# Optimization experiments

Measured on AMD Instinct MI355X. Metric: run time of the kernel, lower is better.

## Reference

```python
import jax, jax.numpy as jnp
import numpy as np

MAX_ITER = 10
EPS = 0.01


def setup_inputs() -> dict:
    key = jax.random.key(0)
    ks = jax.random.split(key, 6)
    B, D, H, O = 4096, 512, 1024, 512
    return {
        "x": jax.random.normal(ks[0], (B, D), jnp.float32),
        "prev_hidden": jax.random.normal(ks[1], (B, H), jnp.float32) * 0.1,
        "prev_ponder": jnp.zeros((B, 1), jnp.float32),
        "prev_steps": jnp.zeros((B, 1), jnp.float32),
        "W_ih": jax.random.normal(ks[2], (H, D + 1), jnp.float32) * 0.02,
        "b_ih": jnp.zeros((H,), jnp.float32),
        "W_hh": jax.random.normal(ks[3], (H, H), jnp.float32) * 0.02,
        "b_hh": jnp.zeros((H,), jnp.float32),
        "W_halt": jax.random.normal(ks[4], (1, H), jnp.float32) * 0.1,
        "b_halt": jnp.zeros((1,), jnp.float32),
        "W_ans": jax.random.normal(ks[5], (O, H), jnp.float32) * 0.02,
        "b_ans": jnp.zeros((O,), jnp.float32),
    }


def reference(x, prev_hidden, prev_ponder, prev_steps,
              W_ih, b_ih, W_hh, b_hh, W_halt, b_halt, W_ans, b_ans):
    B = x.shape[0]
    O = W_ans.shape[0]

    def controller(x_n, s):  # vanilla tanh RNN cell (cfg.MODEL.LSTM=False)
        return jnp.tanh(x_n @ W_ih.T + b_ih + s @ W_hh.T + b_hh)

    def halting_step(carry, inp):
        flag, n = inp  # n is the 1-based loop index (float), flag=1 only at n==1
        s_n, s_acc, y, h, r_n, R, N, steps = carry
        x_n = jnp.concatenate([x, jnp.full((B, 1), flag, x.dtype)], axis=1)
        s_new = controller(x_n, s_n)                       # [B, H]
        h_n = jax.nn.sigmoid(s_new @ W_halt.T + b_halt)    # [B, 1]
        y_n = s_new @ W_ans.T + b_ans                      # [B, O]
        h = h + h_n
        isN = h >= (1.0 - EPS)                             # halted mask (frozen once true)
        p_n = jnp.where(isN, r_n, h_n)                     # remainder at halting step, else h_n
        y = y + p_n * y_n
        s_acc = s_acc + p_n * s_new
        steps = jnp.where(isN, steps, steps + 1.0)
        r_new = jnp.where(isN, jnp.zeros((), x.dtype), 1.0 - h)
        R_new = jnp.where(isN, R, r_new)
        N_new = jnp.where(isN, N, n + 1.0)
        return (s_new, s_acc, y, h, r_new, R_new, N_new, steps), None

    carry0 = (
        prev_hidden,                          # s_n
        jnp.zeros_like(prev_hidden),          # s accumulator
        jnp.zeros((B, O), x.dtype),           # y
        jnp.zeros((B, 1), x.dtype),           # h (halt prob mass)
        jnp.ones((B, 1), x.dtype),            # r_n
        jnp.ones((B, 1), x.dtype),            # R
        jnp.zeros((B, 1), x.dtype),           # N
        prev_steps + 1.0,                     # steps
    )
    ns = jnp.arange(1, MAX_ITER, dtype=x.dtype)
    flags = (ns == 1).astype(x.dtype)
    carry, _ = jax.lax.scan(halting_step, carry0, (flags, ns))
    s_n, s_acc, y, h, r_n, R, N, steps = carry

    # final (remainder) step, flag = 1 only if MAX_ITER == 1
    final_flag = 1.0 if MAX_ITER == 1 else 0.0
    x_n = jnp.concatenate([x, jnp.full((B, 1), final_flag, x.dtype)], axis=1)
    s_new = controller(x_n, s_n)
    y_n = s_new @ W_ans.T + b_ans
    p_n = r_n                                 # remainder (0 for already-halted rows)
    y = y + p_n * y_n
    s_acc = s_acc + p_n * s_new
    ponder_cost = prev_ponder + R + N
    return (y, s_acc, ponder_cost, steps)
```

## Files before the change

### kernel.cpp

```cpp
#include <hip/hip_runtime.h>
#include <cmath>
#include <cstddef>


#define MAX_ITER 10

typedef short bf16x8 __attribute__((ext_vector_type(8)));
typedef float f32x4  __attribute__((ext_vector_type(4)));

__device__ __forceinline__ ushort f2bf(float f) {
    unsigned u = __float_as_uint(f);
    u += 0x7fff + ((u >> 16) & 1);
    return (ushort)(u >> 16);
}
__device__ __forceinline__ float bf2f(ushort b) {
    return __uint_as_float(((unsigned)b) << 16);
}
__device__ __forceinline__ void gld16(const void* g, void* l) {
    __builtin_amdgcn_global_load_lds(
        (const __attribute__((address_space(1))) void*)g,
        (__attribute__((address_space(3))) void*)l, 16, 0, 0);
}

template<int BM, int BN, int MODE>
__device__ __forceinline__ void gemm_body(
    int bx, int by,
    const ushort* __restrict__ ahi, const ushort* __restrict__ alo, int lda,
    const ushort* __restrict__ bhi, const ushort* __restrict__ blo, int ldb,
    int tps, float* __restrict__ Cout, int ldn,
    const float* __restrict__ e0, const float* __restrict__ e1, float flag,
    ushort* __restrict__ shiO, ushort* __restrict__ sloO,
    ushort* smem)
{
    constexpr int FRM = BM / 32;
    constexpr int FRN = BN / 32;
    constexpr int NL  = BM / 32 + BN / 32;
    ushort* As = smem;
    ushort* Bs = smem + 2 * BM * 64;

    const int tid  = threadIdx.x;
    const int lane = tid & 63;
    const int wave = tid >> 6;
    const int lq   = lane & 15;
    const int kh   = lane >> 4;
    const int wr0  = (wave >> 1) * (BM / 2);
    const int wc0  = (wave & 1) * (BN / 2);
    const int m0   = bx * BM;
    const int n0   = by * BN;

    f32x4 acc[FRM][FRN];
#pragma unroll
    for (int r = 0; r < FRM; ++r)
#pragma unroll
        for (int c = 0; c < FRN; ++c) acc[r][c] = (f32x4)0.f;

    const int steps = 3 * tps;

    auto stage = [&](int buf, int t) {
        const int seg = (t >= 2 * tps) ? 2 : ((t >= tps) ? 1 : 0);
        const int k0  = (t - seg * tps) * 64;
        const ushort* aS = (seg == 2) ? alo : ahi;
        const ushort* bS = (seg == 1) ? blo : bhi;
#pragma unroll
        for (int j = 0; j < BM / 32; ++j) {
            int c   = j * 256 + tid;
            int row = c >> 3;
            int kb  = ((c & 7) << 4) ^ ((row & 7) << 4);
            gld16(aS + (size_t)(m0 + row) * lda + k0 + (kb >> 1),
                  As + buf * (BM * 64) + (size_t)(j * 256 + (tid & ~63)) * 8);
        }
#pragma unroll
        for (int j = 0; j < BN / 32; ++j) {
            int c   = j * 256 + tid;
            int row = c >> 3;
            int kb  = ((c & 7) << 4) ^ ((row & 7) << 4);
            gld16(bS + (size_t)(n0 + row) * ldb + k0 + (kb >> 1),
                  Bs + buf * (BN * 64) + (size_t)(j * 256 + (tid & ~63)) * 8);
        }
    };

    stage(0, 0);
    stage(1, 1);

    int cur = 0;
    for (int t = 0; t < steps; ++t) {
        if (t + 1 < steps) __builtin_amdgcn_s_waitcnt(0xF70 | NL);
        else               __builtin_amdgcn_s_waitcnt(0xF70);
        __builtin_amdgcn_sched_barrier(0);
        __builtin_amdgcn_s_barrier();
        __builtin_amdgcn_sched_barrier(0);

        const ushort* Ab = As + cur * (BM * 64);
        const ushort* Bb = Bs + cur * (BN * 64);
#pragma unroll
        for (int kt = 0; kt < 2; ++kt) {
            bf16x8 af[FRM], bfr[FRN];
#pragma unroll
            for (int r = 0; r < FRM; ++r) {
                int row = wr0 + r * 16 + lq;
                int kb  = (kt * 64 + kh * 16) ^ ((row & 7) << 4);
                af[r] = *reinterpret_cast<const bf16x8*>(&Ab[row * 64 + (kb >> 1)]);
            }
#pragma unroll
            for (int c = 0; c < FRN; ++c) {
                int row = wc0 + c * 16 + lq;
                int kb  = (kt * 64 + kh * 16) ^ ((row & 7) << 4);
                bfr[c] = *reinterpret_cast<const bf16x8*>(&Bb[row * 64 + (kb >> 1)]);
            }
            __builtin_amdgcn_s_setprio(1);
#pragma unroll
            for (int r = 0; r < FRM; ++r)
#pragma unroll
                for (int c = 0; c < FRN; ++c)
                    acc[r][c] = __builtin_amdgcn_mfma_f32_16x16x32_bf16(
                        af[r], bfr[c], acc[r][c], 0, 0, 0);
            __builtin_amdgcn_s_setprio(0);
        }
        __builtin_amdgcn_sched_barrier(0);
        __builtin_amdgcn_s_barrier();
        __builtin_amdgcn_sched_barrier(0);
        if (t + 2 < steps) stage(cur, t + 2);
        cur ^= 1;
    }

#pragma unroll
    for (int r = 0; r < FRM; ++r)
#pragma unroll
        for (int c = 0; c < FRN; ++c) {
            const size_t col = n0 + wc0 + c * 16 + lq;
#pragma unroll
            for (int q = 0; q < 4; ++q) {
                const size_t row = m0 + wr0 + r * 16 + kh * 4 + q;
                float v = acc[r][c][q];
                if constexpr (MODE == 0) {
                    v += e0[col] + e1[col];
                    Cout[row * ldn + col] = v;
                } else if constexpr (MODE == 1) {
                    v += e0[row * ldn + col];
                    if (flag != 0.f) v += flag * e1[col];
                    float s = tanhf(v);
                    ushort hb = f2bf(s);
                    ushort lb = f2bf(s - bf2f(hb));
                    shiO[row * ldn + col] = hb;
                    sloO[row * ldn + col] = lb;
                } else {
                    const float pv = e1[row];
                    float* cp = &Cout[row * ldn + col];
                    *cp = fmaf(pv, v + e0[col], *cp);
                }
            }
        }
}

template<int BM, int BN, int MODE>
__global__ __launch_bounds__(256)
void mfma_gemm(const ushort* __restrict__ ahi, const ushort* __restrict__ alo, int lda,
               const ushort* __restrict__ bhi, const ushort* __restrict__ blo, int ldb,
               int tps, float* __restrict__ Cout, int ldn,
               const float* __restrict__ e0, const float* __restrict__ e1,
               float flag, ushort* __restrict__ shiO, ushort* __restrict__ sloO)
{
    __shared__ __align__(16) ushort smem[2 * (BM + BN) * 64];
    gemm_body<BM, BN, MODE>(blockIdx.x, blockIdx.y, ahi, alo, lda, bhi, blo, ldb,
                            tps, Cout, ldn, e0, e1, flag, shiO, sloO, smem);
}

__global__ __launch_bounds__(256)
void merged_gemm(int m1_blocks, int m1_gx, int m2_gx,
                 const ushort* __restrict__ s_hi, const ushort* __restrict__ s_lo,
                 const ushort* __restrict__ whhhi, const ushort* __restrict__ whhlo,
                 int H, int tps,
                 float* __restrict__ xproj, const float* __restrict__ wcol,
                 ushort* __restrict__ o_hi, ushort* __restrict__ o_lo,
                 const ushort* __restrict__ wanshi, const ushort* __restrict__ wanslo,
                 float* __restrict__ out_y, int O,
                 const float* __restrict__ bans, const float* __restrict__ pA)
{
    extern __shared__ ushort smem[];
    const int b = blockIdx.x;
    if (b < m1_blocks) {
        gemm_body<64, 128, 1>(b % m1_gx, b / m1_gx, s_hi, s_lo, H,
                              whhhi, whhlo, H, tps, nullptr, H,
                              xproj, wcol, 0.f, o_hi, o_lo, smem);
    } else {
        const int b2 = b - m1_blocks;
        gemm_body<64, 64, 2>(b2 % m2_gx, b2 / m2_gx, s_hi, s_lo, H,
                             wanshi, wanslo, H, tps, out_y, O,
                             bans, pA, 0.f, nullptr, nullptr, smem);
    }
}

__global__ void init_kernel(float* __restrict__ out_zero, size_t nzero,
                            float* __restrict__ hA, float* __restrict__ rA,
                            float* __restrict__ RA, float* __restrict__ NA,
                            float* __restrict__ stA,
                            const float* __restrict__ prev_steps, int B)
{
    size_t i = (size_t)blockIdx.x * 256 + threadIdx.x;
    if (i < nzero) out_zero[i] = 0.f;
    if (i < (size_t)B) {
        hA[i] = 0.f; rA[i] = 1.f; RA[i] = 1.f; NA[i] = 0.f;
        stA[i] = prev_steps[i] + 1.f;
    }
}

__global__ void split_f32(const float* __restrict__ src,
                          ushort* __restrict__ hi, ushort* __restrict__ lo, size_t n4)
{
    size_t i = (size_t)blockIdx.x * 256 + threadIdx.x;
    if (i < n4) {
        float4 v = reinterpret_cast<const float4*>(src)[i];
        ushort4 h, l;
        h.x = f2bf(v.x); l.x = f2bf(v.x - bf2f(h.x));
        h.y = f2bf(v.y); l.y = f2bf(v.y - bf2f(h.y));
        h.z = f2bf(v.z); l.z = f2bf(v.z - bf2f(h.z));
        h.w = f2bf(v.w); l.w = f2bf(v.w - bf2f(h.w));
        reinterpret_cast<ushort4*>(hi)[i] = h;
        reinterpret_cast<ushort4*>(lo)[i] = l;
    }
}

__global__ void wih_split(const float* __restrict__ Wih,
                          ushort* __restrict__ hi, ushort* __restrict__ lo,
                          float* __restrict__ wcol, int H, int D)
{
    size_t i = (size_t)blockIdx.x * 256 + threadIdx.x;
    if (i < (size_t)H * D) {
        int h = (int)(i / D), d = (int)(i % D);
        float v = Wih[(size_t)h * (D + 1) + d];
        ushort hb = f2bf(v);
        hi[i] = hb; lo[i] = f2bf(v - bf2f(hb));
    }
    if (i < (size_t)H) wcol[i] = Wih[i * (size_t)(D + 1) + D];
}

__global__ __launch_bounds__(256)
void halt_update(const ushort* __restrict__ shi, const ushort* __restrict__ slo,
                 const float* __restrict__ Whalt, const float* __restrict__ bhalt,
                 float* __restrict__ hA, float* __restrict__ rA, float* __restrict__ RA,
                 float* __restrict__ NA, float* __restrict__ stA, float* __restrict__ pA,
                 float* __restrict__ s_acc, float n1, int H, int isFinal)
{
    const int b = blockIdx.x;
    const int tid = threadIdx.x;
    const size_t base = (size_t)b * H;
    const int i = tid * 4;
    ushort4 h4 = *reinterpret_cast<const ushort4*>(shi + base + i);
    ushort4 l4 = *reinterpret_cast<const ushort4*>(slo + base + i);
    float s0 = bf2f(h4.x) + bf2f(l4.x);
    float s1 = bf2f(h4.y) + bf2f(l4.y);
    float s2 = bf2f(h4.z) + bf2f(l4.z);
    float s3 = bf2f(h4.w) + bf2f(l4.w);

    __shared__ float partial[4];
    __shared__ float psh;
    float4 w4 = *reinterpret_cast<const float4*>(Whalt + i);
    float lsum = s0 * w4.x + s1 * w4.y + s2 * w4.z + s3 * w4.w;
#pragma unroll
    for (int off = 32; off > 0; off >>= 1) lsum += __shfl_down(lsum, off, 64);
    if ((tid & 63) == 0) partial[tid >> 6] = lsum;
    __syncthreads();
    if (tid == 0) {
        float pv;
        if (isFinal) {
            pv = rA[b];
        } else {
            float dot = partial[0] + partial[1] + partial[2] + partial[3] + bhalt[0];
            float h_n = 1.f / (1.f + expf(-dot));
            float hh = hA[b] + h_n;
            bool isN = hh >= 0.99f;
            pv = isN ? rA[b] : h_n;
            float r_new = isN ? 0.f : 1.f - hh;
            if (!isN) { RA[b] = r_new; NA[b] = n1; stA[b] += 1.f; }
            hA[b] = hh; rA[b] = r_new; pA[b] = pv;
        }
        psh = pv;
    }
    __syncthreads();
    const float pv = psh;
    if (pv != 0.f) {
        float4* sac = reinterpret_cast<float4*>(s_acc + base + i);
        float4 o = *sac;
        o.x = fmaf(pv, s0, o.x); o.y = fmaf(pv, s1, o.y);
        o.z = fmaf(pv, s2, o.z); o.w = fmaf(pv, s3, o.w);
        *sac = o;
    }
}

__global__ void finalize_kernel(const float* __restrict__ pp, const float* __restrict__ RA,
                                const float* __restrict__ NA, const float* __restrict__ stA,
                                float* __restrict__ pon, float* __restrict__ stp, int B)
{
    int i = blockIdx.x * 256 + threadIdx.x;
    if (i < B) { pon[i] = pp[i] + RA[i] + NA[i]; stp[i] = stA[i]; }
}

extern "C" void kernel_launch(void* const* d_in, const int* in_sizes, int n_in,
                              void* d_out, int out_size, void* d_ws, size_t ws_size,
                              hipStream_t stream)
{
    const float* x     = (const float*)d_in[0];
    const float* ph    = (const float*)d_in[1];
    const float* pp    = (const float*)d_in[2];
    const float* ps    = (const float*)d_in[3];
    const float* Wih   = (const float*)d_in[4];
    const float* bih   = (const float*)d_in[5];
    const float* Whh   = (const float*)d_in[6];
    const float* bhh   = (const float*)d_in[7];
    const float* Whalt = (const float*)d_in[8];
    const float* bhalt = (const float*)d_in[9];
    const float* Wans  = (const float*)d_in[10];
    const float* bans  = (const float*)d_in[11];

    const int B = in_sizes[2];
    const int H = in_sizes[5];
    const int O = in_sizes[11];
    const int D = in_sizes[0] / B;

    float* out_y   = (float*)d_out;
    float* out_sac = out_y + (size_t)B * O;
    float* out_pon = out_sac + (size_t)B * H;
    float* out_stp = out_pon + B;

    char* w = (char*)d_ws;
    float* xproj = (float*)w;  w += (size_t)B * H * 4;
    ushort* shi[2], *slo[2];
    shi[0] = (ushort*)w; w += (size_t)B * H * 2;
    slo[0] = (ushort*)w; w += (size_t)B * H * 2;
    shi[1] = (ushort*)w; w += (size_t)B * H * 2;
    slo[1] = (ushort*)w; w += (size_t)B * H * 2;
    ushort* whhhi = (ushort*)w; w += (size_t)H * H * 2;
    ushort* whhlo = (ushort*)w; w += (size_t)H * H * 2;
    ushort* wanshi = (ushort*)w; w += (size_t)O * H * 2;
    ushort* wanslo = (ushort*)w; w += (size_t)O * H * 2;
    ushort* wihhi = (ushort*)w; w += (size_t)H * D * 2;
    ushort* wihlo = (ushort*)w; w += (size_t)H * D * 2;
    float* wcol = (float*)w; w += (size_t)H * 4;
    float* hA  = (float*)w; w += (size_t)B * 4;
    float* rA  = (float*)w; w += (size_t)B * 4;
    float* RA  = (float*)w; w += (size_t)B * 4;
    float* NA  = (float*)w; w += (size_t)B * 4;
    float* stA = (float*)w; w += (size_t)B * 4;
    float* pA  = (float*)w; w += (size_t)B * 4;

    ushort* xhi = shi[1];
    ushort* xlo = slo[1];

    const size_t nzero = (size_t)B * (O + H);
    init_kernel<<<(unsigned)((nzero + 255) / 256), 256, 0, stream>>>(
        out_y, nzero, hA, rA, RA, NA, stA, ps, B);

    split_f32<<<(unsigned)(((size_t)B * D / 4 + 255) / 256), 256, 0, stream>>>(x, xhi, xlo, (size_t)B * D / 4);
    split_f32<<<(unsigned)(((size_t)B * H / 4 + 255) / 256), 256, 0, stream>>>(ph, shi[0], slo[0], (size_t)B * H / 4);
    split_f32<<<(unsigned)(((size_t)H * H / 4 + 255) / 256), 256, 0, stream>>>(Whh, whhhi, whhlo, (size_t)H * H / 4);
    split_f32<<<(unsigned)(((size_t)O * H / 4 + 255) / 256), 256, 0, stream>>>(Wans, wanshi, wanslo, (size_t)O * H / 4);
    wih_split<<<(unsigned)(((size_t)H * D + 255) / 256), 256, 0, stream>>>(Wih, wihhi, wihlo, wcol, H, D);

    {
        dim3 g(B / 64, H / 128);
        mfma_gemm<64, 128, 0><<<g, 256, 0, stream>>>(
            xhi, xlo, D, wihhi, wihlo, D, D / 64,
            xproj, H, bih, bhh, 0.f, nullptr, nullptr);
    }

    const int m1_gx = B / 64, m1_gy = H / 128;
    const int m2_gx = B / 64, m2_gy = O / 64;
    const int m1_blocks = m1_gx * m1_gy;
    const int m2_blocks = m2_gx * m2_gy;
    const size_t lds_merged = 2u * (64 + 128) * 64 * sizeof(ushort);

    {
        dim3 g(B / 64, H / 128);
        mfma_gemm<64, 128, 1><<<g, 256, 0, stream>>>(
            shi[0], slo[0], H, whhhi, whhlo, H, H / 64,
            nullptr, H, xproj, wcol, 1.f, shi[1], slo[1]);
    }

    int cur = 1;
    for (int t = 1; t < MAX_ITER; t++) {
        halt_update<<<B, 256, 0, stream>>>(
            shi[cur], slo[cur], Whalt, bhalt, hA, rA, RA, NA, stA, pA,
            out_sac, (float)(t + 1), H, 0);
        merged_gemm<<<m1_blocks + m2_blocks, 256, lds_merged, stream>>>(
            m1_blocks, m1_gx, m2_gx,
            shi[cur], slo[cur], whhhi, whhlo, H, H / 64,
            xproj, wcol, shi[cur ^ 1], slo[cur ^ 1],
            wanshi, wanslo, out_y, O, bans, pA);
        cur ^= 1;
    }

    halt_update<<<B, 256, 0, stream>>>(
        shi[cur], slo[cur], Whalt, bhalt, hA, rA, RA, NA, stA, pA,
        out_sac, 0.f, H, 1);
    {
        dim3 g(B / 64, O / 64);
        mfma_gemm<64, 64, 2><<<g, 256, 0, stream>>>(
            shi[cur], slo[cur], H, wanshi, wanslo, H, H / 64,
            out_y, O, bans, rA, 0.f, nullptr, nullptr);
    }

    finalize_kernel<<<(B + 255) / 256, 256, 0, stream>>>(
        pp, RA, NA, stA, out_pon, out_stp, B);
}
```

Before: 860.2 us.

## Hoist answer projection out of loop via linearity, triple-buffer GEMM, store xproj as bf16 split

Relies on the linearity of the answer head: y = s_acc @ W_ans^T + (sum p) * b_ans. The per-step answer GEMM is dropped from the recurrent loop and a single GEMM on the accumulated state runs at the end, with halt_update accumulating the p sum and emitting a hi/lo bf16 split of s_acc. The GEMM pipeline also goes from double to triple buffering, xproj is stored as a bf16 hi/lo pair instead of fp32, and blocks are remapped in an XCD-aware order. Risks include extra LDS per block lowering occupancy and small numeric differences from the reordered accumulation.

```diff
diff --git a/kernel.cpp b/kernel.cpp
--- a/kernel.cpp
+++ b/kernel.cpp
@@ -29,14 +29,15 @@
     const ushort* __restrict__ bhi, const ushort* __restrict__ blo, int ldb,
     int tps, float* __restrict__ Cout, int ldn,
     const float* __restrict__ e0, const float* __restrict__ e1, float flag,
+    const ushort* __restrict__ uA, const ushort* __restrict__ uB,
     ushort* __restrict__ shiO, ushort* __restrict__ sloO,
     ushort* smem)
 {
     constexpr int FRM = BM / 32;
     constexpr int FRN = BN / 32;
-    constexpr int NL  = BM / 32 + BN / 32;
+    constexpr int NL  = (BM + BN) / 32;
     ushort* As = smem;
-    ushort* Bs = smem + 2 * BM * 64;
+    ushort* Bs = smem + 3 * BM * 64;
 
     const int tid  = threadIdx.x;
     const int lane = tid & 63;
@@ -81,10 +82,13 @@
 
     stage(0, 0);
     stage(1, 1);
+    stage(2, 2);
 
     int cur = 0;
     for (int t = 0; t < steps; ++t) {
-        if (t + 1 < steps) __builtin_amdgcn_s_waitcnt(0xF70 | NL);
+        const int rem = steps - 1 - t;
+        if (rem >= 2)      __builtin_amdgcn_s_waitcnt(0xF70 | (2 * NL));
+        else if (rem == 1) __builtin_amdgcn_s_waitcnt(0xF70 | NL);
         else               __builtin_amdgcn_s_waitcnt(0xF70);
         __builtin_amdgcn_sched_barrier(0);
         __builtin_amdgcn_s_barrier();
@@ -119,8 +123,8 @@
         __builtin_amdgcn_sched_barrier(0);
         __builtin_amdgcn_s_barrier();
         __builtin_amdgcn_sched_barrier(0);
-        if (t + 2 < steps) stage(cur, t + 2);
-        cur ^= 1;
+        if (t + 3 < steps) stage(cur, t + 3);
+        cur = (cur == 2) ? 0 : cur + 1;
     }
 
 #pragma unroll
@@ -134,9 +138,12 @@
                 float v = acc[r][c][q];
                 if constexpr (MODE == 0) {
                     v += e0[col] + e1[col];
-                    Cout[row * ldn + col] = v;
+                    ushort hb = f2bf(v);
+                    ushort lb = f2bf(v - bf2f(hb));
+                    shiO[row * ldn + col] = hb;
+                    sloO[row * ldn + col] = lb;
                 } else if constexpr (MODE == 1) {
-                    v += e0[row * ldn + col];
+                    v += bf2f(uA[row * ldn + col]) + bf2f(uB[row * ldn + col]);
                     if (flag != 0.f) v += flag * e1[col];
                     float s = tanhf(v);
                     ushort hb = f2bf(s);
@@ -144,9 +151,7 @@
                     shiO[row * ldn + col] = hb;
                     sloO[row * ldn + col] = lb;
                 } else {
-                    const float pv = e1[row];
-                    float* cp = &Cout[row * ldn + col];
-                    *cp = fmaf(pv, v + e0[col], *cp);
+                    Cout[row * ldn + col] = v + e1[row] * e0[col];
                 }
             }
         }
@@ -154,53 +159,35 @@
 
 template<int BM, int BN, int MODE>
 __global__ __launch_bounds__(256)
-void mfma_gemm(const ushort* __restrict__ ahi, const ushort* __restrict__ alo, int lda,
+void mfma_gemm(int gx,
+               const ushort* __restrict__ ahi, const ushort* __restrict__ alo, int lda,
                const ushort* __restrict__ bhi, const ushort* __restrict__ blo, int ldb,
                int tps, float* __restrict__ Cout, int ldn,
                const float* __restrict__ e0, const float* __restrict__ e1,
-               float flag, ushort* __restrict__ shiO, ushort* __restrict__ sloO)
-{
-    __shared__ __align__(16) ushort smem[2 * (BM + BN) * 64];
-    gemm_body<BM, BN, MODE>(blockIdx.x, blockIdx.y, ahi, alo, lda, bhi, blo, ldb,
-                            tps, Cout, ldn, e0, e1, flag, shiO, sloO, smem);
-}
-
-__global__ __launch_bounds__(256)
-void merged_gemm(int m1_blocks, int m1_gx, int m2_gx,
-                 const ushort* __restrict__ s_hi, const ushort* __restrict__ s_lo,
-                 const ushort* __restrict__ whhhi, const ushort* __restrict__ whhlo,
-                 int H, int tps,
-                 float* __restrict__ xproj, const float* __restrict__ wcol,
-                 ushort* __restrict__ o_hi, ushort* __restrict__ o_lo,
-                 const ushort* __restrict__ wanshi, const ushort* __restrict__ wanslo,
-                 float* __restrict__ out_y, int O,
-                 const float* __restrict__ bans, const float* __restrict__ pA)
-{
-    extern __shared__ ushort smem[];
+               float flag,
+               const ushort* __restrict__ uA, const ushort* __restrict__ uB,
+               ushort* __restrict__ shiO, ushort* __restrict__ sloO)
+{
+    __shared__ __align__(16) ushort smem[3 * (BM + BN) * 64];
+    const int n = gridDim.x;
     const int b = blockIdx.x;
-    if (b < m1_blocks) {
-        gemm_body<64, 128, 1>(b % m1_gx, b / m1_gx, s_hi, s_lo, H,
-                              whhhi, whhlo, H, tps, nullptr, H,
-                              xproj, wcol, 0.f, o_hi, o_lo, smem);
-    } else {
-        const int b2 = b - m1_blocks;
-        gemm_body<64, 64, 2>(b2 % m2_gx, b2 / m2_gx, s_hi, s_lo, H,
-                             wanshi, wanslo, H, tps, out_y, O,
-                             bans, pA, 0.f, nullptr, nullptr, smem);
-    }
-}
-
-__global__ void init_kernel(float* __restrict__ out_zero, size_t nzero,
+    const int w = (b & 7) * (n >> 3) + (b >> 3);
+    gemm_body<BM, BN, MODE>(w % gx, w / gx, ahi, alo, lda, bhi, blo, ldb,
+                            tps, Cout, ldn, e0, e1, flag, uA, uB,
+                            shiO, sloO, smem);
+}
+
+__global__ void init_kernel(float* __restrict__ sacc_zero, size_t nzero,
                             float* __restrict__ hA, float* __restrict__ rA,
                             float* __restrict__ RA, float* __restrict__ NA,
-                            float* __restrict__ stA,
+                            float* __restrict__ stA, float* __restrict__ pAcc,
                             const float* __restrict__ prev_steps, int B)
 {
     size_t i = (size_t)blockIdx.x * 256 + threadIdx.x;
-    if (i < nzero) out_zero[i] = 0.f;
+    if (i < nzero) sacc_zero[i] = 0.f;
     if (i < (size_t)B) {
         hA[i] = 0.f; rA[i] = 1.f; RA[i] = 1.f; NA[i] = 0.f;
-        stA[i] = prev_steps[i] + 1.f;
+        stA[i] = prev_steps[i] + 1.f; pAcc[i] = 0.f;
     }
 }
 
@@ -238,8 +225,11 @@
 void halt_update(const ushort* __restrict__ shi, const ushort* __restrict__ slo,
                  const float* __restrict__ Whalt, const float* __restrict__ bhalt,
                  float* __restrict__ hA, float* __restrict__ rA, float* __restrict__ RA,
-                 float* __restrict__ NA, float* __restrict__ stA, float* __restrict__ pA,
-                 float* __restrict__ s_acc, float n1, int H, int isFinal)
+                 float* __restrict__ NA, float* __restrict__ stA,
+                 float* __restrict__ pAcc,
+                 float* __restrict__ s_acc,
+                 ushort* __restrict__ fsHi, ushort* __restrict__ fsLo,
+                 float n1, int H, int isFinal)
 {
     const int b = blockIdx.x;
     const int tid = threadIdx.x;
@@ -272,18 +262,33 @@
             pv = isN ? rA[b] : h_n;
             float r_new = isN ? 0.f : 1.f - hh;
             if (!isN) { RA[b] = r_new; NA[b] = n1; stA[b] += 1.f; }
-            hA[b] = hh; rA[b] = r_new; pA[b] = pv;
-        }
+            hA[b] = hh; rA[b] = r_new;
+        }
+        pAcc[b] += pv;
         psh = pv;
     }
     __syncthreads();
     const float pv = psh;
-    if (pv != 0.f) {
-        float4* sac = reinterpret_cast<float4*>(s_acc + base + i);
+    float4* sac = reinterpret_cast<float4*>(s_acc + base + i);
+    if (!isFinal) {
+        if (pv != 0.f) {
+            float4 o = *sac;
+            o.x = fmaf(pv, s0, o.x); o.y = fmaf(pv, s1, o.y);
+            o.z = fmaf(pv, s2, o.z); o.w = fmaf(pv, s3, o.w);
+            *sac = o;
+        }
+    } else {
         float4 o = *sac;
         o.x = fmaf(pv, s0, o.x); o.y = fmaf(pv, s1, o.y);
         o.z = fmaf(pv, s2, o.z); o.w = fmaf(pv, s3, o.w);
         *sac = o;
+        ushort4 fh, fl;
+        fh.x = f2bf(o.x); fl.x = f2bf(o.x - bf2f(fh.x));
+        fh.y = f2bf(o.y); fl.y = f2bf(o.y - bf2f(fh.y));
+        fh.z = f2bf(o.z); fl.z = f2bf(o.z - bf2f(fh.z));
+        fh.w = f2bf(o.w); fl.w = f2bf(o.w - bf2f(fh.w));
+        *reinterpret_cast<ushort4*>(fsHi + base + i) = fh;
+        *reinterpret_cast<ushort4*>(fsLo + base + i) = fl;
     }
 }
 
@@ -323,7 +328,8 @@
     float* out_stp = out_pon + B;
 
     char* w = (char*)d_ws;
-    float* xproj = (float*)w;  w += (size_t)B * H * 4;
+    ushort* xpHi = (ushort*)w; w += (size_t)B * H * 2;
+    ushort* xpLo = (ushort*)w; w += (size_t)B * H * 2;
     ushort* shi[2], *slo[2];
     shi[0] = (ushort*)w; w += (size_t)B * H * 2;
     slo[0] = (ushort*)w; w += (size_t)B * H * 2;
@@ -336,19 +342,20 @@
     ushort* wihhi = (ushort*)w; w += (size_t)H * D * 2;
     ushort* wihlo = (ushort*)w; w += (size_t)H * D * 2;
     float* wcol = (float*)w; w += (size_t)H * 4;
-    float* hA  = (float*)w; w += (size_t)B * 4;
-    float* rA  = (float*)w; w += (size_t)B * 4;
-    float* RA  = (float*)w; w += (size_t)B * 4;
-    float* NA  = (float*)w; w += (size_t)B * 4;
-    float* stA = (float*)w; w += (size_t)B * 4;
-    float* pA  = (float*)w; w += (size_t)B * 4;
+    float* hA   = (float*)w; w += (size_t)B * 4;
+    float* rA   = (float*)w; w += (size_t)B * 4;
+    float* RA   = (float*)w; w += (size_t)B * 4;
+    float* NA   = (float*)w; w += (size_t)B * 4;
+    float* stA  = (float*)w; w += (size_t)B * 4;
+    float* pAcc = (float*)w; w += (size_t)B * 4;
 
     ushort* xhi = shi[1];
     ushort* xlo = slo[1];
-
-    const size_t nzero = (size_t)B * (O + H);
-    init_kernel<<<(unsigned)((nzero + 255) / 256), 256, 0, stream>>>(
-        out_y, nzero, hA, rA, RA, NA, stA, ps, B);
+    ushort* sacHi = xpHi;
+    ushort* sacLo = xpLo;
+
+    init_kernel<<<(unsigned)(((size_t)B * H + 255) / 256), 256, 0, stream>>>(
+        out_sac, (size_t)B * H, hA, rA, RA, NA, stA, pAcc, ps, B);
 
     split_f32<<<(unsigned)(((size_t)B * D / 4 + 255) / 256), 256, 0, stream>>>(x, xhi, xlo, (size_t)B * D / 4);
     split_f32<<<(unsigned)(((size_t)B * H / 4 + 255) / 256), 256, 0, stream>>>(ph, shi[0], slo[0], (size_t)B * H / 4);
@@ -356,48 +363,32 @@
     split_f32<<<(unsigned)(((size_t)O * H / 4 + 255) / 256), 256, 0, stream>>>(Wans, wanshi, wanslo, (size_t)O * H / 4);
     wih_split<<<(unsigned)(((size_t)H * D + 255) / 256), 256, 0, stream>>>(Wih, wihhi, wihlo, wcol, H, D);
 
-    {
-        dim3 g(B / 64, H / 128);
-        mfma_gemm<64, 128, 0><<<g, 256, 0, stream>>>(
-            xhi, xlo, D, wihhi, wihlo, D, D / 64,
-            xproj, H, bih, bhh, 0.f, nullptr, nullptr);
-    }
-
-    const int m1_gx = B / 64, m1_gy = H / 128;
-    const int m2_gx = B / 64, m2_gy = O / 64;
-    const int m1_blocks = m1_gx * m1_gy;
-    const int m2_blocks = m2_gx * m2_gy;
-    const size_t lds_merged = 2u * (64 + 128) * 64 * sizeof(ushort);
-
-    {
-        dim3 g(B / 64, H / 128);
-        mfma_gemm<64, 128, 1><<<g, 256, 0, stream>>>(
-            shi[0], slo[0], H, whhhi, whhlo, H, H / 64,
-            nullptr, H, xproj, wcol, 1.f, shi[1], slo[1]);
-    }
+    mfma_gemm<64, 128, 0><<<(B / 64) * (H / 128), 256, 0, stream>>>(
+        B / 64, xhi, xlo, D, wihhi, wihlo, D, D / 64,
+        nullptr, H, bih, bhh, 0.f, nullptr, nullptr, xpHi, xpLo);
+
+    mfma_gemm<64, 128, 1><<<(B / 64) * (H / 128), 256, 0, stream>>>(
+        B / 64, shi[0], slo[0], H, whhhi, whhlo, H, H / 64,
+        nullptr, H, nullptr, wcol, 1.f, xpHi, xpLo, shi[1], slo[1]);
 
     int cur = 1;
     for (int t = 1; t < MAX_ITER; t++) {
         halt_update<<<B, 256, 0, stream>>>(
-            shi[cur], slo[cur], Whalt, bhalt, hA, rA, RA, NA, stA, pA,
-            out_sac, (float)(t + 1), H, 0);
-        merged_gemm<<<m1_blocks + m2_blocks, 256, lds_merged, stream>>>(
-            m1_blocks, m1_gx, m2_gx,
-            shi[cur], slo[cur], whhhi, whhlo, H, H / 64,
-            xproj, wcol, shi[cur ^ 1], slo[cur ^ 1],
-            wanshi, wanslo, out_y, O, bans, pA);
+            shi[cur], slo[cur], Whalt, bhalt, hA, rA, RA, NA, stA, pAcc,
+            out_sac, nullptr, nullptr, (float)(t + 1), H, 0);
+        mfma_gemm<64, 128, 1><<<(B / 64) * (H / 128), 256, 0, stream>>>(
+            B / 64, shi[cur], slo[cur], H, whhhi, whhlo, H, H / 64,
+            nullptr, H, nullptr, wcol, 0.f, xpHi, xpLo, shi[cur ^ 1], slo[cur ^ 1]);
         cur ^= 1;
     }
 
     halt_update<<<B, 256, 0, stream>>>(
-        shi[cur], slo[cur], Whalt, bhalt, hA, rA, RA, NA, stA, pA,
-        out_sac, 0.f, H, 1);
-    {
-        dim3 g(B / 64, O / 64);
-        mfma_gemm<64, 64, 2><<<g, 256, 0, stream>>>(
-            shi[cur], slo[cur], H, wanshi, wanslo, H, H / 64,
-            out_y, O, bans, rA, 0.f, nullptr, nullptr);
-    }
+        shi[cur], slo[cur], Whalt, bhalt, hA, rA, RA, NA, stA, pAcc,
+        out_sac, sacHi, sacLo, 0.f, H, 1);
+
+    mfma_gemm<64, 64, 3><<<(B / 64) * (O / 64), 256, 0, stream>>>(
+        B / 64, sacHi, sacLo, H, wanshi, wanslo, H, H / 64,
+        out_y, O, bans, pAcc, 0.f, nullptr, nullptr, nullptr, nullptr);
 
     finalize_kernel<<<(B + 255) / 256, 256, 0, stream>>>(
         pp, RA, NA, stA, out_pon, out_stp, B);
```

After: 713.6 us. 1.21x faster.
